# Kernel optimization log

Hardware: AMD Instinct MI355X
Metric: run time of the kernel (lower is better)

Reference implementation:

```python
import jax, jax.numpy as jnp
import numpy as np

HEAD_DIM = 64  # config['head_dim']
# dropout_prob=0.1 is a no-op in eval mode; reference computes deterministic attention.

def setup_inputs() -> dict:
    key = jax.random.key(0)
    kq, kk, kv = jax.random.split(key, 3)
    shape = (2, 12, 2048, HEAD_DIM)  # [batch, heads, seq, head_dim]
    Q = jax.random.normal(kq, shape, dtype=jnp.float32)
    K = jax.random.normal(kk, shape, dtype=jnp.float32)
    V = jax.random.normal(kv, shape, dtype=jnp.float32)
    return {"Q": Q, "K": K, "V": V}

def reference(Q, K, V):
    # dot = Q @ K^T / sqrt(head_dim); attn = softmax(dot); X = attn @ V
    scale = 1.0 / np.float32(np.sqrt(HEAD_DIM))
    dot = jnp.einsum('bhqd,bhkd->bhqk', Q, K) * scale  # [B,H,S,S]
    attn = jax.nn.softmax(dot, axis=-1)
    X = jnp.einsum('bhqk,bhkd->bhqd', attn, V)
    return X
```

## Files before the change

### kernel.cpp

```cpp
#include <hip/hip_runtime.h>
#include <hip/hip_bf16.h>

typedef __attribute__((ext_vector_type(8))) short bf16x8;
typedef __attribute__((ext_vector_type(4))) float f32x4;
typedef __attribute__((ext_vector_type(16))) float f32x16;
typedef __attribute__((ext_vector_type(4))) unsigned short u16x4;
typedef __attribute__((ext_vector_type(2))) unsigned int u32x2;
typedef __attribute__((ext_vector_type(4))) unsigned int u32x4;
typedef __attribute__((ext_vector_type(4))) _Float16 f16x4;
typedef __attribute__((ext_vector_type(8))) _Float16 f16x8;
typedef __attribute__((ext_vector_type(2))) __fp16 h16x2;
typedef __attribute__((ext_vector_type(4))) __fp16 h16x4;

#define SEQ 2048
#define HD 64
#define BH 24

__device__ __forceinline__ unsigned bfpack(float a, float b) {
  union { float f; unsigned u; } ua, ub; ua.f = a; ub.f = b;
  return __builtin_amdgcn_perm(ub.u + 0x8000u, ua.u + 0x8000u, 0x07060302u);
}
__device__ __forceinline__ unsigned short f2bf(float f) {
  union { float f; unsigned u; } v; v.f = f;
  unsigned r = v.u + 0x7fffu + ((v.u >> 16) & 1u);
  return (unsigned short)(r >> 16);
}

__global__ __launch_bounds__(256) void prep_kv(const float* __restrict__ K,
                                               const float* __restrict__ V,
                                               unsigned* __restrict__ Kb,
                                               _Float16* __restrict__ Vt) {
  __shared__ _Float16 t[64 * 68];
  const int bid = blockIdx.x;
  const int sb = bid >> 3;
  const int bh = (bid & 7) * 3 + (sb >> 5);
  const int k0 = (sb & 31) * 64;
  const int tid = threadIdx.x;

  const float4* ks = (const float4*)(K + ((size_t)bh * SEQ + k0) * HD);
  unsigned* kd = Kb + ((size_t)bh * SEQ + k0) * (HD / 2);
#pragma unroll
  for (int i = 0; i < 4; ++i) {
    int f = tid + i * 256;
    float4 v = ks[f];
    u32x2 o;
    o.x = bfpack(v.x, v.y);
    o.y = bfpack(v.z, v.w);
    *(u32x2*)&kd[f * 2] = o;
  }

  const float4* vs = (const float4*)(V + ((size_t)bh * SEQ + k0) * HD);
#pragma unroll
  for (int i = 0; i < 4; ++i) {
    int f = tid + i * 256;
    int k = f >> 4, cg = f & 15;
    float4 v = vs[k * 16 + cg];
    int dg = cg * 4;
    t[(dg + 0) * 68 + k] = (_Float16)v.x;
    t[(dg + 1) * 68 + k] = (_Float16)v.y;
    t[(dg + 2) * 68 + k] = (_Float16)v.z;
    t[(dg + 3) * 68 + k] = (_Float16)v.w;
  }
  __syncthreads();
  int d = tid >> 2, kg = (tid & 3) * 16;
  _Float16* g = Vt + ((size_t)(bh * 64 + d)) * SEQ + k0 + kg;
#pragma unroll
  for (int r = 0; r < 4; ++r) {
    f16x4 x = *(f16x4*)&t[d * 68 + kg + r * 4];
    *(f16x4*)&g[r * 4] = x;
  }
}

__global__ __launch_bounds__(256, 3) void attn_main(const float* __restrict__ Q,
                                                    const unsigned short* __restrict__ Kb,
                                                    const _Float16* __restrict__ Vt,
                                                    float* __restrict__ O) {
  __shared__ unsigned short kv[3][8192];

  const int tid  = threadIdx.x;
  const int lane = tid & 63;
  const int w    = tid >> 6;
  const int quad = lane >> 4;
  const int n    = lane & 15;
  const bool hi16 = (lane & 16) != 0;

  const int bid = blockIdx.x;
  const int sb = bid >> 3;
  const int bh = (bid & 7) * 3 + (sb >> 5);
  const int q0 = (sb & 31) * 64;

  const float qscale = 0.125f * 1.44269504088896f;

  bf16x8 qf[4][2];
#pragma unroll
  for (int u = 0; u < 4; ++u) {
    const float* qb = Q + ((size_t)bh * SEQ + q0 + u * 16 + n) * HD;
#pragma unroll
    for (int h = 0; h < 2; ++h) {
      float4 a = *(const float4*)(qb + h * 32 + quad * 8);
      float4 b = *(const float4*)(qb + h * 32 + quad * 8 + 4);
      u32x4 pk;
      pk.x = bfpack(a.x * qscale, a.y * qscale);
      pk.y = bfpack(a.z * qscale, a.w * qscale);
      pk.z = bfpack(b.x * qscale, b.y * qscale);
      pk.w = bfpack(b.z * qscale, b.w * qscale);
      qf[u][h] = __builtin_bit_cast(bf16x8, pk);
    }
  }

  const unsigned short* Kbase = Kb + (size_t)bh * SEQ * HD;
  const unsigned short* Vbase = (const unsigned short*)(Vt + (size_t)bh * HD * SEQ);
  const unsigned short* ksrc[2];
  const unsigned short* vsrc[2];
  int soff[2];
#pragma unroll
  for (int i = 0; i < 2; ++i) {
    int s = i * 256 + tid;
    int r = s >> 3, p = s & 7, G = p ^ (r & 7);
    ksrc[i] = Kbase + r * HD + G * 8;
    vsrc[i] = Vbase + (size_t)r * SEQ + G * 8;
    soff[i] = s * 8;
  }

#define DMA_TO(buf_, it_)                                                                 \
  {                                                                                       \
    unsigned short* db_ = &kv[buf_][0];                                                   \
    _Pragma("unroll")                                                                     \
    for (int i_ = 0; i_ < 2; ++i_) {                                                      \
      __builtin_amdgcn_global_load_lds(                                                   \
          (const __attribute__((address_space(1))) void*)(ksrc[i_] + (size_t)(it_) * 4096), \
          (__attribute__((address_space(3))) void*)(db_ + soff[i_]), 16, 0, 0);           \
      __builtin_amdgcn_global_load_lds(                                                   \
          (const __attribute__((address_space(1))) void*)(vsrc[i_] + (size_t)(it_) * 64), \
          (__attribute__((address_space(3))) void*)(db_ + 4096 + soff[i_]), 16, 0, 0);    \
    }                                                                                     \
    asm volatile("" ::: "memory");                                                        \
  }

  f32x16 oacc[2][2];
#pragma unroll
  for (int d_ = 0; d_ < 2; ++d_)
#pragma unroll
    for (int g_ = 0; g_ < 2; ++g_) oacc[d_][g_] = (f32x16)(0.f);
  float lsum[4] = {0.f, 0.f, 0.f, 0.f};

  int ro[2];
#pragma unroll
  for (int h = 0; h < 2; ++h) ro[h] = n * 64 + (((h * 4 + quad) ^ (n & 7)) * 8);
  int vaoff[2];
#pragma unroll
  for (int d_ = 0; d_ < 2; ++d_)
    vaoff[d_] = (d_ * 32 + (lane & 31)) * 64 + (((w * 2 + (lane >> 5)) ^ (lane & 7)) * 8);

#define COMPUTE(buf_)                                                                     \
  {                                                                                       \
    const unsigned short* kb = &kv[buf_][0];                                              \
    const _Float16* vb = (const _Float16*)(kb + 4096);                                    \
    f32x4 s[4] = {{0,0,0,0},{0,0,0,0},{0,0,0,0},{0,0,0,0}};                               \
    _Pragma("unroll")                                                                     \
    for (int h = 0; h < 2; ++h) {                                                         \
      bf16x8 a = *(const bf16x8*)&kb[w * 1024 + ro[h]];                                   \
      _Pragma("unroll")                                                                   \
      for (int u = 0; u < 4; ++u)                                                         \
        s[u] = __builtin_amdgcn_mfma_f32_16x16x32_bf16(a, qf[u][h], s[u], 0, 0, 0);       \
    }                                                                                     \
    f16x8 va0 = *(const f16x8*)&vb[vaoff[0]];                                             \
    f16x8 va1 = *(const f16x8*)&vb[vaoff[1]];                                             \
    unsigned pc0[4], pc1[4];                                                              \
    _Pragma("unroll")                                                                     \
    for (int u = 0; u < 4; ++u) {                                                         \
      float e0 = __builtin_amdgcn_exp2f(s[u][0]);                                         \
      float e1 = __builtin_amdgcn_exp2f(s[u][1]);                                         \
      float e2 = __builtin_amdgcn_exp2f(s[u][2]);                                         \
      float e3 = __builtin_amdgcn_exp2f(s[u][3]);                                         \
      lsum[u] += (e0 + e1) + (e2 + e3);                                                   \
      h16x2 a_ = __builtin_amdgcn_cvt_pkrtz(e0, e1);                                      \
      h16x2 b_ = __builtin_amdgcn_cvt_pkrtz(e2, e3);                                      \
      pc0[u] = __builtin_bit_cast(unsigned, a_);                                          \
      pc1[u] = __builtin_bit_cast(unsigned, b_);                                          \
    }                                                                                     \
    _Pragma("unroll")                                                                     \
    for (int qg = 0; qg < 2; ++qg) {                                                      \
      unsigned A0 = pc0[qg * 2], A1 = pc0[qg * 2 + 1];                                    \
      unsigned B0 = pc1[qg * 2], B1 = pc1[qg * 2 + 1];                                    \
      unsigned S0 = (unsigned)__builtin_amdgcn_ds_swizzle((int)A0, 0x401F);               \
      unsigned S1 = (unsigned)__builtin_amdgcn_ds_swizzle((int)A1, 0x401F);               \
      unsigned T0 = (unsigned)__builtin_amdgcn_ds_swizzle((int)B0, 0x401F);               \
      unsigned T1 = (unsigned)__builtin_amdgcn_ds_swizzle((int)B1, 0x401F);               \
      u32x4 pw;                                                                           \
      pw.x = hi16 ? S1 : A0;                                                              \
      pw.y = hi16 ? T1 : B0;                                                              \
      pw.z = hi16 ? A1 : S0;                                                              \
      pw.w = hi16 ? B1 : T0;                                                              \
      f16x8 pb = __builtin_bit_cast(f16x8, pw);                                           \
      oacc[0][qg] = __builtin_amdgcn_mfma_f32_32x32x16_f16(va0, pb, oacc[0][qg], 0, 0, 0);\
      oacc[1][qg] = __builtin_amdgcn_mfma_f32_32x32x16_f16(va1, pb, oacc[1][qg], 0, 0, 0);\
    }                                                                                     \
  }

  DMA_TO(0, 0);
  DMA_TO(1, 1);

  int bc = 0;
  int bd = 2;
  for (int it = 0; it < 31; ++it) {
    asm volatile("s_waitcnt vmcnt(4)\n\ts_barrier" ::: "memory");
    if (it < 30) DMA_TO(bd, it + 2);
    COMPUTE(bc);
    bc = (bc == 2) ? 0 : bc + 1;
    bd = (bd == 2) ? 0 : bd + 1;
  }
  asm volatile("s_waitcnt vmcnt(0)\n\ts_barrier" ::: "memory");
  COMPUTE(bc);

#undef DMA_TO
#undef COMPUTE

#pragma unroll
  for (int u = 0; u < 4; ++u) {
    lsum[u] += __shfl_xor(lsum[u], 16);
    lsum[u] += __shfl_xor(lsum[u], 32);
  }

  float* red = (float*)&kv[0][0];
  float* lred = red + 2 * 4096;

  __syncthreads();
  if (w & 1) {
    int sl = w >> 1;
#pragma unroll
    for (int f = 0; f < 4; ++f) {
      const int d_ = f >> 1, g_ = f & 1;
#pragma unroll
      for (int rq = 0; rq < 4; ++rq) {
        f32x4 ch = {oacc[d_][g_][rq * 4 + 0], oacc[d_][g_][rq * 4 + 1],
                    oacc[d_][g_][rq * 4 + 2], oacc[d_][g_][rq * 4 + 3]};
        *(f32x4*)&red[sl * 4096 + (f * 4 + rq) * 256 + lane * 4] = ch;
      }
    }
#pragma unroll
    for (int u = 0; u < 4; ++u) lred[sl * 256 + u * 64 + lane] = lsum[u];
  }
  __syncthreads();
  if (!(w & 1)) {
    int sl = w >> 1;
#pragma unroll
    for (int f = 0; f < 4; ++f) {
      const int d_ = f >> 1, g_ = f & 1;
#pragma unroll
      for (int rq = 0; rq < 4; ++rq) {
        f32x4 ch = *(f32x4*)&red[sl * 4096 + (f * 4 + rq) * 256 + lane * 4];
        oacc[d_][g_][rq * 4 + 0] += ch.x;
        oacc[d_][g_][rq * 4 + 1] += ch.y;
        oacc[d_][g_][rq * 4 + 2] += ch.z;
        oacc[d_][g_][rq * 4 + 3] += ch.w;
      }
    }
#pragma unroll
    for (int u = 0; u < 4; ++u) lsum[u] += lred[sl * 256 + u * 64 + lane];
  }
  __syncthreads();
  if (w == 2) {
#pragma unroll
    for (int f = 0; f < 4; ++f) {
      const int d_ = f >> 1, g_ = f & 1;
#pragma unroll
      for (int rq = 0; rq < 4; ++rq) {
        f32x4 ch = {oacc[d_][g_][rq * 4 + 0], oacc[d_][g_][rq * 4 + 1],
                    oacc[d_][g_][rq * 4 + 2], oacc[d_][g_][rq * 4 + 3]};
        *(f32x4*)&red[4096 + (f * 4 + rq) * 256 + lane * 4] = ch;
      }
    }
#pragma unroll
    for (int u = 0; u < 4; ++u) lred[256 + u * 64 + lane] = lsum[u];
  }
  __syncthreads();
  if (w == 0) {
#pragma unroll
    for (int f = 0; f < 4; ++f) {
      const int d_ = f >> 1, g_ = f & 1;
#pragma unroll
      for (int rq = 0; rq < 4; ++rq) {
        f32x4 ch = *(f32x4*)&red[4096 + (f * 4 + rq) * 256 + lane * 4];
        oacc[d_][g_][rq * 4 + 0] += ch.x;
        oacc[d_][g_][rq * 4 + 1] += ch.y;
        oacc[d_][g_][rq * 4 + 2] += ch.z;
        oacc[d_][g_][rq * 4 + 3] += ch.w;
      }
    }
    float L[4];
#pragma unroll
    for (int u = 0; u < 4; ++u) L[u] = lsum[u] + lred[256 + u * 64 + lane];
    const int l31 = lane & 31, hb = lane >> 5;
#pragma unroll
    for (int g_ = 0; g_ < 2; ++g_) {
      const float iv = (lane & 16) ? 1.0f / L[g_ * 2 + 1] : 1.0f / L[g_ * 2];
#pragma unroll
      for (int d_ = 0; d_ < 2; ++d_) {
        float* og = O + ((size_t)bh * SEQ + q0 + g_ * 32 + l31) * HD + d_ * 32 + 4 * hb;
#pragma unroll
        for (int rq = 0; rq < 4; ++rq) {
          f32x4 r = {oacc[d_][g_][rq * 4 + 0] * iv, oacc[d_][g_][rq * 4 + 1] * iv,
                     oacc[d_][g_][rq * 4 + 2] * iv, oacc[d_][g_][rq * 4 + 3] * iv};
          *(f32x4*)(og + 8 * rq) = r;
        }
      }
    }
  }
}

#define F_QT 128
#define F_KT 64
#define F_LD 72

__global__ __launch_bounds__(512) void attn_fwd(const float* __restrict__ Q,
                                                const float* __restrict__ K,
                                                const float* __restrict__ V,
                                                float* __restrict__ O) {
  __shared__ unsigned short sm[(F_QT + F_KT + HD + 8 * 16) * F_LD];
  unsigned short* Qs = sm;
  unsigned short* Ks = Qs + F_QT * F_LD;
  unsigned short* Vt = Ks + F_KT * F_LD;
  unsigned short* Ps = Vt + HD * F_LD;

  const int tid = threadIdx.x, lane = tid & 63, wv = tid >> 6;
  const int quad = lane >> 4, n = lane & 15;
  const int bh = blockIdx.y, q0 = blockIdx.x * F_QT;
  const float* Qg = Q + ((size_t)bh * SEQ + q0) * HD;
  const float* Kg = K + (size_t)bh * SEQ * HD;
  const float* Vg = V + (size_t)bh * SEQ * HD;
  float* Og = O + ((size_t)bh * SEQ + q0) * HD;
  const float qscale = 0.125f * 1.44269504088896f;

#pragma unroll
  for (int i = 0; i < 4; ++i) {
    int f = tid + i * 512;
    int row = f >> 4, cg = f & 15;
    float4 qv = ((const float4*)Qg)[row * 16 + cg];
    u16x4 h;
    h.x = f2bf(qv.x * qscale); h.y = f2bf(qv.y * qscale);
    h.z = f2bf(qv.z * qscale); h.w = f2bf(qv.w * qscale);
    *(u16x4*)&Qs[row * F_LD + cg * 4] = h;
  }
  __syncthreads();
  bf16x8 qf0 = *(const bf16x8*)&Qs[(wv * 16 + n) * F_LD + quad * 8];
  bf16x8 qf1 = *(const bf16x8*)&Qs[(wv * 16 + n) * F_LD + 32 + quad * 8];
  f32x4 o[4] = {{0,0,0,0},{0,0,0,0},{0,0,0,0},{0,0,0,0}};
  float mrow[4] = {-1e30f,-1e30f,-1e30f,-1e30f};
  float lrow[4] = {0.f,0.f,0.f,0.f};
  unsigned short* Pw = Ps + wv * 16 * F_LD;

  for (int it = 0; it < SEQ / F_KT; ++it) {
    __syncthreads();
    const float* Ktg = Kg + (size_t)it * F_KT * HD;
    const float* Vtg = Vg + (size_t)it * F_KT * HD;
#pragma unroll
    for (int i = 0; i < 2; ++i) {
      int f = tid + i * 512;
      int row = f >> 4, cg = f & 15;
      float4 kvv = ((const float4*)Ktg)[row * 16 + cg];
      u16x4 hk;
      hk.x = f2bf(kvv.x); hk.y = f2bf(kvv.y); hk.z = f2bf(kvv.z); hk.w = f2bf(kvv.w);
      *(u16x4*)&Ks[row * F_LD + cg * 4] = hk;
      float4 vv = ((const float4*)Vtg)[row * 16 + cg];
      Vt[(cg * 4 + 0) * F_LD + row] = f2bf(vv.x);
      Vt[(cg * 4 + 1) * F_LD + row] = f2bf(vv.y);
      Vt[(cg * 4 + 2) * F_LD + row] = f2bf(vv.z);
      Vt[(cg * 4 + 3) * F_LD + row] = f2bf(vv.w);
    }
    __syncthreads();
    f32x4 s[4];
#pragma unroll
    for (int t = 0; t < 4; ++t) {
      bf16x8 b0 = *(const bf16x8*)&Ks[(t * 16 + n) * F_LD + quad * 8];
      bf16x8 b1 = *(const bf16x8*)&Ks[(t * 16 + n) * F_LD + 32 + quad * 8];
      f32x4 c = {0,0,0,0};
      c = __builtin_amdgcn_mfma_f32_16x16x32_bf16(qf0, b0, c, 0, 0, 0);
      c = __builtin_amdgcn_mfma_f32_16x16x32_bf16(qf1, b1, c, 0, 0, 0);
      s[t] = c;
    }
    float mnew[4], alpha[4], rsum[4];
#pragma unroll
    for (int r = 0; r < 4; ++r) {
      float ml = fmaxf(fmaxf(s[0][r], s[1][r]), fmaxf(s[2][r], s[3][r]));
      ml = fmaxf(ml, __shfl_xor(ml, 1));
      ml = fmaxf(ml, __shfl_xor(ml, 2));
      ml = fmaxf(ml, __shfl_xor(ml, 4));
      ml = fmaxf(ml, __shfl_xor(ml, 8));
      mnew[r] = fmaxf(mrow[r], ml);
      alpha[r] = __builtin_amdgcn_exp2f(mrow[r] - mnew[r]);
      mrow[r] = mnew[r];
      rsum[r] = 0.f;
    }
#pragma unroll
    for (int t = 0; t < 4; ++t)
#pragma unroll
      for (int r = 0; r < 4; ++r) {
        float p = __builtin_amdgcn_exp2f(s[t][r] - mnew[r]);
        rsum[r] += p;
        Pw[(quad * 4 + r) * F_LD + t * 16 + n] = f2bf(p);
      }
#pragma unroll
    for (int r = 0; r < 4; ++r) {
      float rs = rsum[r];
      rs += __shfl_xor(rs, 1); rs += __shfl_xor(rs, 2);
      rs += __shfl_xor(rs, 4); rs += __shfl_xor(rs, 8);
      lrow[r] = lrow[r] * alpha[r] + rs;
      o[0][r] *= alpha[r]; o[1][r] *= alpha[r];
      o[2][r] *= alpha[r]; o[3][r] *= alpha[r];
    }
    asm volatile("s_waitcnt lgkmcnt(0)" ::: "memory");
    bf16x8 p0 = *(const bf16x8*)&Pw[n * F_LD + quad * 8];
    bf16x8 p1 = *(const bf16x8*)&Pw[n * F_LD + 32 + quad * 8];
#pragma unroll
    for (int t = 0; t < 4; ++t) {
      bf16x8 v0 = *(const bf16x8*)&Vt[(t * 16 + n) * F_LD + quad * 8];
      bf16x8 v1 = *(const bf16x8*)&Vt[(t * 16 + n) * F_LD + 32 + quad * 8];
      o[t] = __builtin_amdgcn_mfma_f32_16x16x32_bf16(p0, v0, o[t], 0, 0, 0);
      o[t] = __builtin_amdgcn_mfma_f32_16x16x32_bf16(p1, v1, o[t], 0, 0, 0);
    }
  }
  float inv[4];
#pragma unroll
  for (int r = 0; r < 4; ++r) inv[r] = 1.0f / lrow[r];
#pragma unroll
  for (int t = 0; t < 4; ++t)
#pragma unroll
    for (int r = 0; r < 4; ++r)
      Og[(wv * 16 + quad * 4 + r) * HD + t * 16 + n] = o[t][r] * inv[r];
}

extern "C" void kernel_launch(void* const* d_in, const int* in_sizes, int n_in,
                              void* d_out, int out_size, void* d_ws, size_t ws_size,
                              hipStream_t stream) {
  const float* Q = (const float*)d_in[0];
  const float* K = (const float*)d_in[1];
  const float* V = (const float*)d_in[2];
  float* O = (float*)d_out;

  const size_t mat = (size_t)BH * SEQ * HD;
  const size_t need = 2 * mat * sizeof(unsigned short);

  if (ws_size >= need) {
    unsigned short* Kb = (unsigned short*)d_ws;
    _Float16* Vt = (_Float16*)(Kb + mat);
    prep_kv<<<dim3(SEQ / 64 * BH), 256, 0, stream>>>(K, V, (unsigned*)Kb, Vt);
    attn_main<<<dim3(BH * SEQ / 64), 256, 0, stream>>>(Q, Kb, Vt, O);
  } else {
    attn_fwd<<<dim3(SEQ / F_QT, BH), 512, 0, stream>>>(Q, K, V, O);
  }
}
```

Baseline: 121.5 us.

## Use v_permlane16_swap for P shuffle and change block-to-head mapping

```diff
diff --git a/kernel.cpp b/kernel.cpp
--- a/kernel.cpp
+++ b/kernel.cpp
@@ -31,10 +31,8 @@
                                                unsigned* __restrict__ Kb,
                                                _Float16* __restrict__ Vt) {
   __shared__ _Float16 t[64 * 68];
-  const int bid = blockIdx.x;
-  const int sb = bid >> 3;
-  const int bh = (bid & 7) * 3 + (sb >> 5);
-  const int k0 = (sb & 31) * 64;
+  const int bh = blockIdx.y;
+  const int k0 = blockIdx.x * 64;
   const int tid = threadIdx.x;
 
   const float4* ks = (const float4*)(K + ((size_t)bh * SEQ + k0) * HD);
@@ -82,12 +80,9 @@
   const int w    = tid >> 6;
   const int quad = lane >> 4;
   const int n    = lane & 15;
-  const bool hi16 = (lane & 16) != 0;
-
-  const int bid = blockIdx.x;
-  const int sb = bid >> 3;
-  const int bh = (bid & 7) * 3 + (sb >> 5);
-  const int q0 = (sb & 31) * 64;
+
+  const int bh = blockIdx.x;
+  const int q0 = blockIdx.y * 64;
 
   const float qscale = 0.125f * 1.44269504088896f;
 
@@ -183,15 +178,17 @@
     for (int qg = 0; qg < 2; ++qg) {                                                      \
       unsigned A0 = pc0[qg * 2], A1 = pc0[qg * 2 + 1];                                    \
       unsigned B0 = pc1[qg * 2], B1 = pc1[qg * 2 + 1];                                    \
-      unsigned S0 = (unsigned)__builtin_amdgcn_ds_swizzle((int)A0, 0x401F);               \
-      unsigned S1 = (unsigned)__builtin_amdgcn_ds_swizzle((int)A1, 0x401F);               \
-      unsigned T0 = (unsigned)__builtin_amdgcn_ds_swizzle((int)B0, 0x401F);               \
-      unsigned T1 = (unsigned)__builtin_amdgcn_ds_swizzle((int)B1, 0x401F);               \
+                \
+                \
+                \
+                \
+      asm("v_permlane16_swap_b32 %0, %1" : "+v"(A0), "+v"(A1));                           \
+      asm("v_permlane16_swap_b32 %0, %1" : "+v"(B0), "+v"(B1));                           \
       u32x4 pw;                                                                           \
-      pw.x = hi16 ? S1 : A0;                                                              \
-      pw.y = hi16 ? T1 : B0;                                                              \
-      pw.z = hi16 ? A1 : S0;                                                              \
-      pw.w = hi16 ? B1 : T0;                                                              \
+      pw.x = A0;                                                                          \
+      pw.y = B0;                                                                          \
+      pw.z = A1;                                                                          \
+      pw.w = B1;                                                                          \
       f16x8 pb = __builtin_bit_cast(f16x8, pw);                                           \
       oacc[0][qg] = __builtin_amdgcn_mfma_f32_32x32x16_f16(va0, pb, oacc[0][qg], 0, 0, 0);\
       oacc[1][qg] = __builtin_amdgcn_mfma_f32_32x32x16_f16(va1, pb, oacc[1][qg], 0, 0, 0);\
@@ -444,8 +441,8 @@
   if (ws_size >= need) {
     unsigned short* Kb = (unsigned short*)d_ws;
     _Float16* Vt = (_Float16*)(Kb + mat);
-    prep_kv<<<dim3(SEQ / 64 * BH), 256, 0, stream>>>(K, V, (unsigned*)Kb, Vt);
-    attn_main<<<dim3(BH * SEQ / 64), 256, 0, stream>>>(Q, Kb, Vt, O);
+    prep_kv<<<dim3(SEQ / 64, BH), 256, 0, stream>>>(K, V, (unsigned*)Kb, Vt);
+    attn_main<<<dim3(BH, SEQ / 64), 256, 0, stream>>>(Q, Kb, Vt, O);
   } else {
     attn_fwd<<<dim3(SEQ / F_QT, BH), 512, 0, stream>>>(Q, K, V, O);
   }
```

After: 132.9 us. 9.4% more time.
